# Optimization experiments

Measured on AMD Instinct MI355X. Metric: run time of the kernel, lower is better.

## Reference

```python
import jax, jax.numpy as jnp
import numpy as np

N = 8192
F_IN = 512
F_OUT = 64
ALPHA = 0.2  # LeakyReLU negative slope
NEG_INF = -9e15


def setup_inputs() -> dict:
    key = jax.random.key(0)
    k1, k2, k3, k4 = jax.random.split(key, 4)
    inp = jax.random.normal(k1, (N, F_IN), dtype=jnp.float32)
    adj = jax.random.randint(k2, (N, N), 0, 2, dtype=jnp.int32)
    W = jax.random.normal(k3, (F_IN, F_OUT), dtype=jnp.float32) * 0.05
    a = jax.random.normal(k4, (2 * F_OUT, 1), dtype=jnp.float32) * 0.05
    return {"inp": inp, "adj": adj, "W": W, "a": a}


def reference(inp, adj, W, a):
    # h = W(inp): [N, F_OUT]
    h = inp @ W
    # a([h_i || h_j]) decomposes exactly into a1.h_i + a2.h_j, avoiding the
    # [N*N, 2F] concat tensor while computing identical math.
    f1 = h @ a[:F_OUT]        # [N, 1] source-node term
    f2 = h @ a[F_OUT:]        # [N, 1] target-node term
    e = jax.nn.leaky_relu(f1 + f2.T, negative_slope=ALPHA)  # [N, N]
    masked = jnp.where(adj > 0, e, jnp.float32(NEG_INF))
    attention = jax.nn.softmax(masked, axis=1)  # dropout is no-op at inference
    h_prime = attention @ h   # [N, F_OUT]
    return jax.nn.elu(h_prime)  # concat=True branch
```

## Files before the change

### kernel.cpp

```cpp
#include <hip/hip_runtime.h>

#define NN   8192
#define FIN  512
#define FOUT 64
#define KT   256

typedef __attribute__((ext_vector_type(8))) short short8;
typedef __attribute__((ext_vector_type(4))) float floatx4;

__device__ __forceinline__ unsigned f2bf_u(float f) {
  union { float f; unsigned u; } v; v.f = f;
  return (v.u + 0x7fffu + ((v.u >> 16) & 1u)) >> 16;
}
__device__ __forceinline__ unsigned pack2(float a, float b) {
  return f2bf_u(a) | (f2bf_u(b) << 16);
}

union U8 { uint4 u; short8 s; };

__global__ __launch_bounds__(256) void k1_gemm_h(
    const float* __restrict__ inp, const float* __restrict__ W,
    const float* __restrict__ a,
    float* __restrict__ f1, float* __restrict__ f2,
    unsigned short* __restrict__ hT)
{
  __shared__ unsigned short wt[64][520];
  __shared__ float hsm[16][65];
  __shared__ float alds[2 * FOUT];

  const int tid   = threadIdx.x;
  const int rbase = blockIdx.x * 16;
  if (tid < 2 * FOUT) alds[tid] = a[tid];

  {
    const float4* Wv = (const float4*)W;
#pragma unroll
    for (int j = 0; j < 32; ++j) {
      const int i  = j * 256 + tid;
      const int k  = i >> 4;
      const int c4 = (i & 15) * 4;
      float4 f = Wv[i];
      wt[c4 + 0][k] = (unsigned short)f2bf_u(f.x);
      wt[c4 + 1][k] = (unsigned short)f2bf_u(f.y);
      wt[c4 + 2][k] = (unsigned short)f2bf_u(f.z);
      wt[c4 + 3][k] = (unsigned short)f2bf_u(f.w);
    }
  }

  const int lane = tid & 63;
  const int wv   = tid >> 6;
  const int l15  = lane & 15;
  const int q    = lane >> 4;

  const float* ap = inp + (size_t)(rbase + l15) * FIN + q * 8;

  float4 Ab[2][4];
#pragma unroll
  for (int b = 0; b < 2; ++b) {
    Ab[b][0] = *(const float4*)(ap + b * 64);
    Ab[b][1] = *(const float4*)(ap + b * 64 + 4);
    Ab[b][2] = *(const float4*)(ap + b * 64 + 32);
    Ab[b][3] = *(const float4*)(ap + b * 64 + 36);
  }

  floatx4 acc = {0.f, 0.f, 0.f, 0.f};
  __syncthreads();

#pragma unroll
  for (int t = 0; t < 8; ++t) {
    const int cur = t & 1;
    U8 c0, c1;
    c0.u = make_uint4(pack2(Ab[cur][0].x, Ab[cur][0].y), pack2(Ab[cur][0].z, Ab[cur][0].w),
                      pack2(Ab[cur][1].x, Ab[cur][1].y), pack2(Ab[cur][1].z, Ab[cur][1].w));
    c1.u = make_uint4(pack2(Ab[cur][2].x, Ab[cur][2].y), pack2(Ab[cur][2].z, Ab[cur][2].w),
                      pack2(Ab[cur][3].x, Ab[cur][3].y), pack2(Ab[cur][3].z, Ab[cur][3].w));
    if (t < 6) {
      const float* an = ap + (t + 2) * 64;
      Ab[cur][0] = *(const float4*)(an);
      Ab[cur][1] = *(const float4*)(an + 4);
      Ab[cur][2] = *(const float4*)(an + 32);
      Ab[cur][3] = *(const float4*)(an + 36);
    }
    const unsigned short* wrow = &wt[wv * 16 + l15][t * 64 + q * 8];
    short8 b0 = *(const short8*)(wrow);
    short8 b1 = *(const short8*)(wrow + 32);
    acc = __builtin_amdgcn_mfma_f32_16x16x32_bf16(c0.s, b0, acc, 0, 0, 0);
    acc = __builtin_amdgcn_mfma_f32_16x16x32_bf16(c1.s, b1, acc, 0, 0, 0);
  }

  const int m0 = q * 4;
  const int n  = wv * 16 + l15;
#pragma unroll
  for (int rg = 0; rg < 4; ++rg) hsm[m0 + rg][n] = acc[rg];
  *(uint2*)&hT[(size_t)n * NN + rbase + m0] =
      make_uint2(pack2(acc[0], acc[1]), pack2(acc[2], acc[3]));

  __syncthreads();
  if (tid < 16) {
    float s1 = 0.f, s2 = 0.f;
#pragma unroll 8
    for (int c = 0; c < FOUT; ++c) {
      float hv = hsm[tid][c];
      s1 += hv * alds[c];
      s2 += hv * alds[FOUT + c];
    }
    f1[rbase + tid] = s1;
    f2[rbase + tid] = s2;
  }
}

#define GAT_W4(FV, AV, P0, P1)                                              \
  { float e0 = f1v + FV.x; e0 = fmaxf(e0, 0.2f * e0);                       \
    float e1 = f1v + FV.y; e1 = fmaxf(e1, 0.2f * e1);                       \
    float e2 = f1v + FV.z; e2 = fmaxf(e2, 0.2f * e2);                       \
    float e3 = f1v + FV.w; e3 = fmaxf(e3, 0.2f * e3);                       \
    float x0 = AV.x ? __expf(e0) : 0.f;                                     \
    float x1 = AV.y ? __expf(e1) : 0.f;                                     \
    float x2 = AV.z ? __expf(e2) : 0.f;                                     \
    float x3 = AV.w ? __expf(e3) : 0.f;                                     \
    lsum += (x0 + x1) + (x2 + x3);                                          \
    P0 = pack2(x0, x1); P1 = pack2(x2, x3); }

#define K2_ITER(IT, ACUR, ANXT, BUF)                                        \
  {                                                                          \
    if ((IT) < 31) {   \
      const int* apf = arow + ((IT) + 1) * KT;                               \
      ANXT[0] = *(const int4*)(apf);                                         \
      ANXT[1] = *(const int4*)(apf + 4);                                     \
      ANXT[2] = *(const int4*)(apf + 8);                                     \
      ANXT[3] = *(const int4*)(apf + 12);                                    \
    }                                                                        \
    unsigned p0, p1, p2, p3, p4, p5, p6, p7;                                 \
    GAT_W4(F[0], ACUR[0], p0, p1)                                            \
    GAT_W4(F[1], ACUR[1], p2, p3)                                            \
    GAT_W4(F[2], ACUR[2], p4, p5)                                            \
    GAT_W4(F[3], ACUR[3], p6, p7)                                            \
    *(uint4*)&wlds[BUF][r][c16]     = make_uint4(p0, p1, p2, p3);            \
    *(uint4*)&wlds[BUF][r][c16 + 8] = make_uint4(p4, p5, p6, p7);            \
    if ((IT) < 31) {       \
      const float* fpf = frow + ((IT) + 1) * KT;                             \
      F[0] = *(const float4*)(fpf);                                          \
      F[1] = *(const float4*)(fpf + 4);                                      \
      F[2] = *(const float4*)(fpf + 8);                                      \
      F[3] = *(const float4*)(fpf + 12);                                     \
    }                                                                        \
    asm volatile("s_waitcnt lgkmcnt(0)" ::: "memory");     \
    __builtin_amdgcn_s_barrier();       \
    _Pragma("unroll")                                                        \
    for (int ks = 0; ks < 8; ++ks) {                                         \
      short8 af = *(const short8*)&wlds[BUF][l15][ks * 32 + q * 8];          \
      acc = __builtin_amdgcn_mfma_f32_16x16x32_bf16(af, Hf[ks], acc, 0, 0, 0); \
    }                                                                        \
    if ((IT) < 31) {                \
      const unsigned short* hpf = hrow + ((IT) + 1) * KT;                    \
      _Pragma("unroll")                                                      \
      for (int ks = 0; ks < 8; ++ks) Hf[ks] = *(const short8*)(hpf + ks * 32); \
    }                                                                        \
  }

__global__ __launch_bounds__(256) void k2_attn(
    const int* __restrict__ adj,
    const float* __restrict__ f1g, const float* __restrict__ f2g,
    const unsigned short* __restrict__ hT,
    float* __restrict__ out)
{
  __shared__ unsigned short wlds[2][16][264];
  __shared__ float lred[16][17];
  __shared__ float linv_s[16];

  const int tid   = threadIdx.x;
  const int rbase = blockIdx.x * 16;
  const int lane  = tid & 63;
  const int wv    = tid >> 6;
  const int l15   = lane & 15;
  const int q     = lane >> 4;

  const int r   = tid >> 4;
  const int c16 = (tid & 15) * 16;
  const float f1v = f1g[rbase + r];
  const int* arow   = adj + (size_t)(rbase + r) * NN + c16;
  const float* frow = f2g + c16;
  const unsigned short* hrow = hT + (size_t)(wv * 16 + l15) * NN + q * 8;

  floatx4 acc = {0.f, 0.f, 0.f, 0.f};
  float lsum = 0.f;

  int4 Aa[4], Az[4];
  float4 F[4];
  short8 Hf[8];

  Aa[0] = *(const int4*)(arow);
  Aa[1] = *(const int4*)(arow + 4);
  Aa[2] = *(const int4*)(arow + 8);
  Aa[3] = *(const int4*)(arow + 12);
  F[0] = *(const float4*)(frow);
  F[1] = *(const float4*)(frow + 4);
  F[2] = *(const float4*)(frow + 8);
  F[3] = *(const float4*)(frow + 12);
#pragma unroll
  for (int ks = 0; ks < 8; ++ks) Hf[ks] = *(const short8*)(hrow + ks * 32);

  for (int it = 0; it < 32; it += 2) {
    K2_ITER(it,     Aa, Az, 0)
    K2_ITER(it + 1, Az, Aa, 1)
  }

  lred[r][tid & 15] = lsum;
  __syncthreads();
  if (tid < 16) {
    float s = 0.f;
#pragma unroll
    for (int i = 0; i < 16; ++i) s += lred[tid][i];
    linv_s[tid] = 1.f / s;
  }
  __syncthreads();

  const int m0 = q * 4;
  const int n2 = wv * 16 + l15;
#pragma unroll
  for (int rg = 0; rg < 4; ++rg) {
    float v = acc[rg] * linv_s[m0 + rg];
    v = (v > 0.f) ? v : (__expf(v) - 1.f);
    out[(size_t)(rbase + m0 + rg) * FOUT + n2] = v;
  }
}

extern "C" void kernel_launch(void* const* d_in, const int* in_sizes, int n_in,
                              void* d_out, int out_size, void* d_ws, size_t ws_size,
                              hipStream_t stream) {
  (void)in_sizes; (void)n_in; (void)out_size; (void)ws_size;
  const float* inp = (const float*)d_in[0];
  const int*   adj = (const int*)d_in[1];
  const float* W   = (const float*)d_in[2];
  const float* a   = (const float*)d_in[3];
  float* out = (float*)d_out;

  float* f1 = (float*)d_ws;
  float* f2 = f1 + NN;
  unsigned short* hT = (unsigned short*)(f2 + NN);

  k1_gemm_h<<<NN / 16, 256, 0, stream>>>(inp, W, a, f1, f2, hT);
  k2_attn<<<NN / 16, 256, 0, stream>>>(adj, f1, f2, hT, out);
}
```

Measured before the change: 390.9 us.

## Split attention columns across two blocks and combine partial sums

Doubles the k2 grid by giving each block half of the neighbour columns for its 16 rows. Each block writes an unnormalized partial accumulator and a partial row sum, and a new combine kernel adds the two halves, normalizes and applies ELU. It also sets a launch-bounds occupancy hint of four blocks. The aim is more blocks in flight on the many CUs (512 blocks was low) so the adjacency stream hides latency better, at the cost of an extra launch and a partial-buffer round trip.

Measured after the change: 412.8 us. 5.6% more time.

```diff
diff --git a/kernel.cpp b/kernel.cpp
--- a/kernel.cpp
+++ b/kernel.cpp
@@ -123,7 +123,7 @@
 
 #define K2_ITER(IT, ACUR, ANXT, BUF)                                        \
   {                                                                          \
-    if ((IT) < 31) {   \
+    if ((IT) < 15) {   \
       const int* apf = arow + ((IT) + 1) * KT;                               \
       ANXT[0] = *(const int4*)(apf);                                         \
       ANXT[1] = *(const int4*)(apf + 4);                                     \
@@ -137,7 +137,7 @@
     GAT_W4(F[3], ACUR[3], p6, p7)                                            \
     *(uint4*)&wlds[BUF][r][c16]     = make_uint4(p0, p1, p2, p3);            \
     *(uint4*)&wlds[BUF][r][c16 + 8] = make_uint4(p4, p5, p6, p7);            \
-    if ((IT) < 31) {       \
+    if ((IT) < 15) {       \
       const float* fpf = frow + ((IT) + 1) * KT;                             \
       F[0] = *(const float4*)(fpf);                                          \
       F[1] = *(const float4*)(fpf + 4);                                      \
@@ -151,25 +151,26 @@
       short8 af = *(const short8*)&wlds[BUF][l15][ks * 32 + q * 8];          \
       acc = __builtin_amdgcn_mfma_f32_16x16x32_bf16(af, Hf[ks], acc, 0, 0, 0); \
     }                                                                        \
-    if ((IT) < 31) {                \
+    if ((IT) < 15) {                \
       const unsigned short* hpf = hrow + ((IT) + 1) * KT;                    \
       _Pragma("unroll")                                                      \
       for (int ks = 0; ks < 8; ++ks) Hf[ks] = *(const short8*)(hpf + ks * 32); \
     }                                                                        \
   }
 
-__global__ __launch_bounds__(256) void k2_attn(
+__global__ __launch_bounds__(256, 4) void k2_attn_part(
     const int* __restrict__ adj,
     const float* __restrict__ f1g, const float* __restrict__ f2g,
     const unsigned short* __restrict__ hT,
-    float* __restrict__ out)
+    float* __restrict__ pacc, float* __restrict__ psum)
 {
   __shared__ unsigned short wlds[2][16][264];
   __shared__ float lred[16][17];
-  __shared__ float linv_s[16];
 
   const int tid   = threadIdx.x;
-  const int rbase = blockIdx.x * 16;
+  const int bid   = blockIdx.x;
+  const int rbase = (bid >> 1) * 16;
+  const int cbase = (bid & 1) * 4096;
   const int lane  = tid & 63;
   const int wv    = tid >> 6;
   const int l15   = lane & 15;
@@ -178,9 +179,9 @@
   const int r   = tid >> 4;
   const int c16 = (tid & 15) * 16;
   const float f1v = f1g[rbase + r];
-  const int* arow   = adj + (size_t)(rbase + r) * NN + c16;
-  const float* frow = f2g + c16;
-  const unsigned short* hrow = hT + (size_t)(wv * 16 + l15) * NN + q * 8;
+  const int* arow   = adj + (size_t)(rbase + r) * NN + cbase + c16;
+  const float* frow = f2g + cbase + c16;
+  const unsigned short* hrow = hT + (size_t)(wv * 16 + l15) * NN + cbase + q * 8;
 
   floatx4 acc = {0.f, 0.f, 0.f, 0.f};
   float lsum = 0.f;
@@ -200,7 +201,7 @@
 #pragma unroll
   for (int ks = 0; ks < 8; ++ks) Hf[ks] = *(const short8*)(hrow + ks * 32);
 
-  for (int it = 0; it < 32; it += 2) {
+  for (int it = 0; it < 16; it += 2) {
     K2_ITER(it,     Aa, Az, 0)
     K2_ITER(it + 1, Az, Aa, 1)
   }
@@ -211,18 +212,37 @@
     float s = 0.f;
 #pragma unroll
     for (int i = 0; i < 16; ++i) s += lred[tid][i];
-    linv_s[tid] = 1.f / s;
-  }
-  __syncthreads();
+    psum[bid * 16 + tid] = s;
+  }
 
   const int m0 = q * 4;
   const int n2 = wv * 16 + l15;
 #pragma unroll
-  for (int rg = 0; rg < 4; ++rg) {
-    float v = acc[rg] * linv_s[m0 + rg];
-    v = (v > 0.f) ? v : (__expf(v) - 1.f);
-    out[(size_t)(rbase + m0 + rg) * FOUT + n2] = v;
-  }
+  for (int rg = 0; rg < 4; ++rg)
+    pacc[(size_t)bid * (16 * FOUT) + (m0 + rg) * FOUT + n2] = acc[rg];
+}
+
+__global__ __launch_bounds__(256) void k3_combine(
+    const float* __restrict__ pacc, const float* __restrict__ psum,
+    float* __restrict__ out)
+{
+  const int idx = blockIdx.x * 256 + threadIdx.x;
+  const int row = idx >> 4;
+  const int f4  = (idx & 15) * 4;
+  const int rb  = row >> 4;
+  const int sub = row & 15;
+
+  const float4 vA = *(const float4*)&pacc[(size_t)(2 * rb + 0) * (16 * FOUT) + sub * FOUT + f4];
+  const float4 vB = *(const float4*)&pacc[(size_t)(2 * rb + 1) * (16 * FOUT) + sub * FOUT + f4];
+  const float inv = 1.f / (psum[(2 * rb + 0) * 16 + sub] + psum[(2 * rb + 1) * 16 + sub]);
+
+  float4 o;
+  float v;
+  v = (vA.x + vB.x) * inv; o.x = (v > 0.f) ? v : (__expf(v) - 1.f);
+  v = (vA.y + vB.y) * inv; o.y = (v > 0.f) ? v : (__expf(v) - 1.f);
+  v = (vA.z + vB.z) * inv; o.z = (v > 0.f) ? v : (__expf(v) - 1.f);
+  v = (vA.w + vB.w) * inv; o.w = (v > 0.f) ? v : (__expf(v) - 1.f);
+  *(float4*)&out[(size_t)row * FOUT + f4] = o;
 }
 
 extern "C" void kernel_launch(void* const* d_in, const int* in_sizes, int n_in,
@@ -238,7 +258,10 @@
   float* f1 = (float*)d_ws;
   float* f2 = f1 + NN;
   unsigned short* hT = (unsigned short*)(f2 + NN);
+  float* pacc = (float*)(hT + (size_t)FOUT * NN);
+  float* psum = pacc + (size_t)1024 * 16 * FOUT;
 
   k1_gemm_h<<<NN / 16, 256, 0, stream>>>(inp, W, a, f1, f2, hT);
-  k2_attn<<<NN / 16, 256, 0, stream>>>(adj, f1, f2, hT, out);
-}
+  k2_attn_part<<<NN / 16 * 2, 256, 0, stream>>>(adj, f1, f2, hT, pacc, psum);
+  k3_combine<<<NN * FOUT / 4 / 256, 256, 0, stream>>>(pacc, psum, out);
+}
```

## Split attention K dimension across waves with register-resident softmax weights

Applied to the files above, without the earlier changes.

The attention kernel now gives each wave a quarter of the neighbour dimension. Each lane computes the exp weights directly in the MFMA A-operand register layout and feeds them to four MFMAs covering all 64 output features, so the per-tile LDS staging and block-wide barriers are gone. The f2 vector is copied into shared memory once per block, and partial accumulators and row sums are combined across waves through shared memory at the end. In exchange, each block reads the full 32 KB f2 vector and every wave loads all four hT feature groups, and the launch bounds now ask for 4 blocks per SM (occupancy hint).

After: 416.4 us. 1.07x slower.

```diff
diff --git a/kernel.cpp b/kernel.cpp
--- a/kernel.cpp
+++ b/kernel.cpp
@@ -3,7 +3,6 @@
 #define NN   8192
 #define FIN  512
 #define FOUT 64
-#define KT   256
 
 typedef __attribute__((ext_vector_type(8))) short short8;
 typedef __attribute__((ext_vector_type(4))) float floatx4;
@@ -109,64 +108,49 @@
   }
 }
 
-#define GAT_W4(FV, AV, P0, P1)                                              \
-  { float e0 = f1v + FV.x; e0 = fmaxf(e0, 0.2f * e0);                       \
-    float e1 = f1v + FV.y; e1 = fmaxf(e1, 0.2f * e1);                       \
-    float e2 = f1v + FV.z; e2 = fmaxf(e2, 0.2f * e2);                       \
-    float e3 = f1v + FV.w; e3 = fmaxf(e3, 0.2f * e3);                       \
-    float x0 = AV.x ? __expf(e0) : 0.f;                                     \
-    float x1 = AV.y ? __expf(e1) : 0.f;                                     \
-    float x2 = AV.z ? __expf(e2) : 0.f;                                     \
-    float x3 = AV.w ? __expf(e3) : 0.f;                                     \
-    lsum += (x0 + x1) + (x2 + x3);                                          \
-    P0 = pack2(x0, x1); P1 = pack2(x2, x3); }
-
-#define K2_ITER(IT, ACUR, ANXT, BUF)                                        \
+#define K2_BODY(S, AC0, AC1, AN0, AN1)                                       \
   {                                                                          \
-    if ((IT) < 31) {   \
-      const int* apf = arow + ((IT) + 1) * KT;                               \
-      ANXT[0] = *(const int4*)(apf);                                         \
-      ANXT[1] = *(const int4*)(apf + 4);                                     \
-      ANXT[2] = *(const int4*)(apf + 8);                                     \
-      ANXT[3] = *(const int4*)(apf + 12);                                    \
+    if ((S) < 63) {             \
+      const int* apf = arow + ((S) + 1) * 32;                                \
+      AN0 = *(const int4*)(apf);                                             \
+      AN1 = *(const int4*)(apf + 4);                                         \
     }                                                                        \
-    unsigned p0, p1, p2, p3, p4, p5, p6, p7;                                 \
-    GAT_W4(F[0], ACUR[0], p0, p1)                                            \
-    GAT_W4(F[1], ACUR[1], p2, p3)                                            \
-    GAT_W4(F[2], ACUR[2], p4, p5)                                            \
-    GAT_W4(F[3], ACUR[3], p6, p7)                                            \
-    *(uint4*)&wlds[BUF][r][c16]     = make_uint4(p0, p1, p2, p3);            \
-    *(uint4*)&wlds[BUF][r][c16 + 8] = make_uint4(p4, p5, p6, p7);            \
-    if ((IT) < 31) {       \
-      const float* fpf = frow + ((IT) + 1) * KT;                             \
-      F[0] = *(const float4*)(fpf);                                          \
-      F[1] = *(const float4*)(fpf + 4);                                      \
-      F[2] = *(const float4*)(fpf + 8);                                      \
-      F[3] = *(const float4*)(fpf + 12);                                     \
-    }                                                                        \
-    asm volatile("s_waitcnt lgkmcnt(0)" ::: "memory");     \
-    __builtin_amdgcn_s_barrier();       \
-    _Pragma("unroll")                                                        \
-    for (int ks = 0; ks < 8; ++ks) {                                         \
-      short8 af = *(const short8*)&wlds[BUF][l15][ks * 32 + q * 8];          \
-      acc = __builtin_amdgcn_mfma_f32_16x16x32_bf16(af, Hf[ks], acc, 0, 0, 0); \
-    }                                                                        \
-    if ((IT) < 31) {                \
-      const unsigned short* hpf = hrow + ((IT) + 1) * KT;                    \
-      _Pragma("unroll")                                                      \
-      for (int ks = 0; ks < 8; ++ks) Hf[ks] = *(const short8*)(hpf + ks * 32); \
-    }                                                                        \
-  }
-
-__global__ __launch_bounds__(256) void k2_attn(
+    short8 h0 = *(const short8*)(hp0 + (S) * 32);            \
+    short8 h1 = *(const short8*)(hp1 + (S) * 32);                            \
+    short8 h2 = *(const short8*)(hp2 + (S) * 32);                            \
+    short8 h3 = *(const short8*)(hp3 + (S) * 32);                            \
+    const float* fp = fbase + (S) * 32;                                      \
+    float4 g0 = *(const float4*)(fp);               \
+    float4 g1 = *(const float4*)(fp + 4);                                    \
+    float e, w0, w1, w2, w3, w4, w5, w6, w7;                                 \
+    e = f1v + g0.x; e = fmaxf(e, 0.2f * e); w0 = AC0.x ? __expf(e) : 0.f;    \
+    e = f1v + g0.y; e = fmaxf(e, 0.2f * e); w1 = AC0.y ? __expf(e) : 0.f;    \
+    e = f1v + g0.z; e = fmaxf(e, 0.2f * e); w2 = AC0.z ? __expf(e) : 0.f;    \
+    e = f1v + g0.w; e = fmaxf(e, 0.2f * e); w3 = AC0.w ? __expf(e) : 0.f;    \
+    e = f1v + g1.x; e = fmaxf(e, 0.2f * e); w4 = AC1.x ? __expf(e) : 0.f;    \
+    e = f1v + g1.y; e = fmaxf(e, 0.2f * e); w5 = AC1.y ? __expf(e) : 0.f;    \
+    e = f1v + g1.z; e = fmaxf(e, 0.2f * e); w6 = AC1.z ? __expf(e) : 0.f;    \
+    e = f1v + g1.w; e = fmaxf(e, 0.2f * e); w7 = AC1.w ? __expf(e) : 0.f;    \
+    lsum += ((w0 + w1) + (w2 + w3)) + ((w4 + w5) + (w6 + w7));               \
+    U8 af;                                                                   \
+    af.u = make_uint4(pack2(w0, w1), pack2(w2, w3),                          \
+                      pack2(w4, w5), pack2(w6, w7));                         \
+    acc0 = __builtin_amdgcn_mfma_f32_16x16x32_bf16(af.s, h0, acc0, 0, 0, 0); \
+    acc1 = __builtin_amdgcn_mfma_f32_16x16x32_bf16(af.s, h1, acc1, 0, 0, 0); \
+    acc2 = __builtin_amdgcn_mfma_f32_16x16x32_bf16(af.s, h2, acc2, 0, 0, 0); \
+    acc3 = __builtin_amdgcn_mfma_f32_16x16x32_bf16(af.s, h3, acc3, 0, 0, 0); \
+  }
+
+__global__ __launch_bounds__(256, 4) void k2_attn(
     const int* __restrict__ adj,
     const float* __restrict__ f1g, const float* __restrict__ f2g,
     const unsigned short* __restrict__ hT,
     float* __restrict__ out)
 {
-  __shared__ unsigned short wlds[2][16][264];
-  __shared__ float lred[16][17];
-  __shared__ float linv_s[16];
+  __shared__ union SMU {
+    float f2s[NN];
+    struct { float pacc[4][16][65]; float ls[4][16][5]; } red;
+  } sm;
 
   const int tid   = threadIdx.x;
   const int rbase = blockIdx.x * 16;
@@ -175,54 +159,68 @@
   const int l15   = lane & 15;
   const int q     = lane >> 4;
 
-  const int r   = tid >> 4;
-  const int c16 = (tid & 15) * 16;
-  const float f1v = f1g[rbase + r];
-  const int* arow   = adj + (size_t)(rbase + r) * NN + c16;
-  const float* frow = f2g + c16;
-  const unsigned short* hrow = hT + (size_t)(wv * 16 + l15) * NN + q * 8;
-
-  floatx4 acc = {0.f, 0.f, 0.f, 0.f};
+  {
+    const float4* fv = (const float4*)f2g;
+    float4* s4 = (float4*)sm.f2s;
+#pragma unroll
+    for (int j = 0; j < 8; ++j) s4[j * 256 + tid] = fv[j * 256 + tid];
+  }
+  const float f1v = f1g[rbase + l15];
+  __syncthreads();
+
+  const int k0 = wv * 2048 + q * 8;
+  const int* arow = adj + (size_t)(rbase + l15) * NN + k0;
+  const unsigned short* hp0 = hT + (size_t)(0 * 16 + l15) * NN + k0;
+  const unsigned short* hp1 = hT + (size_t)(1 * 16 + l15) * NN + k0;
+  const unsigned short* hp2 = hT + (size_t)(2 * 16 + l15) * NN + k0;
+  const unsigned short* hp3 = hT + (size_t)(3 * 16 + l15) * NN + k0;
+  const float* fbase = sm.f2s + k0;
+
+  floatx4 acc0 = {0.f, 0.f, 0.f, 0.f};
+  floatx4 acc1 = {0.f, 0.f, 0.f, 0.f};
+  floatx4 acc2 = {0.f, 0.f, 0.f, 0.f};
+  floatx4 acc3 = {0.f, 0.f, 0.f, 0.f};
   float lsum = 0.f;
 
-  int4 Aa[4], Az[4];
-  float4 F[4];
-  short8 Hf[8];
-
-  Aa[0] = *(const int4*)(arow);
-  Aa[1] = *(const int4*)(arow + 4);
-  Aa[2] = *(const int4*)(arow + 8);
-  Aa[3] = *(const int4*)(arow + 12);
-  F[0] = *(const float4*)(frow);
-  F[1] = *(const float4*)(frow + 4);
-  F[2] = *(const float4*)(frow + 8);
-  F[3] = *(const float4*)(frow + 12);
-#pragma unroll
-  for (int ks = 0; ks < 8; ++ks) Hf[ks] = *(const short8*)(hrow + ks * 32);
-
-  for (int it = 0; it < 32; it += 2) {
-    K2_ITER(it,     Aa, Az, 0)
-    K2_ITER(it + 1, Az, Aa, 1)
-  }
-
-  lred[r][tid & 15] = lsum;
-  __syncthreads();
-  if (tid < 16) {
-    float s = 0.f;
-#pragma unroll
-    for (int i = 0; i < 16; ++i) s += lred[tid][i];
-    linv_s[tid] = 1.f / s;
-  }
-  __syncthreads();
-
-  const int m0 = q * 4;
-  const int n2 = wv * 16 + l15;
+  int4 Aa0, Aa1, Ba0, Ba1;
+  Aa0 = *(const int4*)(arow);
+  Aa1 = *(const int4*)(arow + 4);
+
+  for (int s = 0; s < 64; s += 2) {
+    K2_BODY(s,     Aa0, Aa1, Ba0, Ba1)
+    K2_BODY(s + 1, Ba0, Ba1, Aa0, Aa1)
+  }
+
+  __syncthreads();
 #pragma unroll
   for (int rg = 0; rg < 4; ++rg) {
-    float v = acc[rg] * linv_s[m0 + rg];
-    v = (v > 0.f) ? v : (__expf(v) - 1.f);
-    out[(size_t)(rbase + m0 + rg) * FOUT + n2] = v;
-  }
+    sm.red.pacc[wv][q * 4 + rg][0 * 16 + l15] = acc0[rg];
+    sm.red.pacc[wv][q * 4 + rg][1 * 16 + l15] = acc1[rg];
+    sm.red.pacc[wv][q * 4 + rg][2 * 16 + l15] = acc2[rg];
+    sm.red.pacc[wv][q * 4 + rg][3 * 16 + l15] = acc3[rg];
+  }
+  sm.red.ls[wv][l15][q] = lsum;
+  __syncthreads();
+
+  const int r  = tid >> 4;
+  const int f0 = (tid & 15) * 4;
+  float s0 = 0.f, s1 = 0.f, s2 = 0.f, s3 = 0.f, rs = 0.f;
+#pragma unroll
+  for (int w = 0; w < 4; ++w) {
+    s0 += sm.red.pacc[w][r][f0 + 0];
+    s1 += sm.red.pacc[w][r][f0 + 1];
+    s2 += sm.red.pacc[w][r][f0 + 2];
+    s3 += sm.red.pacc[w][r][f0 + 3];
+    rs += ((sm.red.ls[w][r][0] + sm.red.ls[w][r][1]) +
+           (sm.red.ls[w][r][2] + sm.red.ls[w][r][3]));
+  }
+  const float inv = 1.f / rs;
+  float4 o; float v;
+  v = s0 * inv; o.x = (v > 0.f) ? v : (__expf(v) - 1.f);
+  v = s1 * inv; o.y = (v > 0.f) ? v : (__expf(v) - 1.f);
+  v = s2 * inv; o.z = (v > 0.f) ? v : (__expf(v) - 1.f);
+  v = s3 * inv; o.w = (v > 0.f) ? v : (__expf(v) - 1.f);
+  *(float4*)&out[(size_t)(rbase + r) * FOUT + f0] = o;
 }
 
 extern "C" void kernel_launch(void* const* d_in, const int* in_sizes, int n_in,
```
